# Optimization experiments

Measured on AMD Instinct MI355X. Metric: run time of the kernel, lower is better.

The kernel has to match this reference:

```python
import jax, jax.numpy as jnp
import numpy as np
from jax import lax

T, K, D = 2097152, 8, 4
LOG_2PI = float(np.log(2.0 * np.pi))


def setup_inputs() -> dict:
    key = jax.random.key(0)
    k1, k2, k3, k4 = jax.random.split(key, 4)
    return {
        "x_seq": jax.random.normal(k1, (T, D), dtype=jnp.float32),
        "unnormalized_trans": jax.random.normal(k2, (K, K), dtype=jnp.float32),
        "unnormalized_pi": jax.random.normal(k3, (K,), dtype=jnp.float32),
        "means": jax.random.normal(k4, (K, D), dtype=jnp.float32) * 0.01,
        "log_std": jnp.zeros((K, D), dtype=jnp.float32),
    }


def reference(x_seq, unnormalized_trans, unnormalized_pi, means, log_std):
    # Row-stochastic transition / initial distributions in log space
    log_trans = jax.nn.log_softmax(unnormalized_trans, axis=-1)  # [K, K]
    log_pi = jax.nn.log_softmax(unnormalized_pi, axis=-1)        # [K]

    # Diagonal-Gaussian log emission densities: [T, K]
    std = jnp.exp(log_std)                                        # [K, D]
    z = (x_seq[:, None, :] - means[None, :, :]) / std[None, :, :]  # [T, K, D]
    log_em = jnp.sum(-0.5 * LOG_2PI - log_std[None] - 0.5 * z * z, axis=-1)  # [T, K]

    # Forward algorithm in log space (strictly sequential recurrence)
    alpha0 = log_pi + log_em[0]  # [K]

    def step(alpha, em_t):
        # alpha[i] + log_trans[i, j], logsumexp over source state i
        alpha = em_t + jax.scipy.special.logsumexp(alpha[:, None] + log_trans, axis=0)
        return alpha, None

    alpha, _ = lax.scan(step, alpha0, log_em[1:])
    return jax.scipy.special.logsumexp(alpha, axis=0)
```

## Files before the change

kernel.cpp:

```cpp
#include <hip/hip_runtime.h>
#include <math.h>

#define T_LEN 2097152
#define K 8
#define D 4
#define CHUNK 8
#define TPB 64
#define NBLK (T_LEN / (CHUNK * TPB))
#define MS4 19
#define NMID 16
#define MPM (NBLK / NMID)

typedef float f2 __attribute__((ext_vector_type(2)));

__device__ __forceinline__ f2 fma2(f2 a, f2 b, f2 c) { return __builtin_elementwise_fma(a, b, c); }
__device__ __forceinline__ f2 max2(f2 a, f2 b) { return __builtin_elementwise_max(a, b); }
__device__ __forceinline__ f2 splat(float s) { f2 r; r.x = s; r.y = s; return r; }


__device__ __forceinline__ float4* matp4(float* lm, int li) {
    return reinterpret_cast<float4*>(lm) + li * MS4 + ((li >> 1) & 3);
}

__device__ __forceinline__ void renorm2(f2 M[K][4], float& shift) {
    f2 m2 = max2(max2(M[0][0], M[0][1]), max2(M[0][2], M[0][3]));
#pragma unroll
    for (int i = 1; i < K; ++i)
        m2 = max2(m2, max2(max2(M[i][0], M[i][1]), max2(M[i][2], M[i][3])));
    float mx = fmaxf(m2.x, m2.y);
    int ex = (__float_as_int(mx) >> 23) & 255;
    float scale = __int_as_float((254 - ex) << 23);
    shift += (float)(ex - 127);
    f2 sc = splat(scale);
#pragma unroll
    for (int i = 0; i < K; ++i)
#pragma unroll
        for (int jj = 0; jj < 4; ++jj) M[i][jj] = M[i][jj] * sc;
}

__device__ __forceinline__ void store_mat(float* lm, int li, const f2 M[K][4]) {
    float4* dst = matp4(lm, li);
#pragma unroll
    for (int i = 0; i < K; ++i) {
        float4 w0, w1;
        w0.x = M[i][0].x; w0.y = M[i][0].y; w0.z = M[i][1].x; w0.w = M[i][1].y;
        w1.x = M[i][2].x; w1.y = M[i][2].y; w1.z = M[i][3].x; w1.w = M[i][3].y;
        dst[i * 2] = w0;
        dst[i * 2 + 1] = w1;
    }
}

__device__ __forceinline__ void combine8(float* lm, float* lsh, int li, int ri, int i) {
    const float4* Lb = matp4(lm, li);
    const float4* Rb = matp4(lm, ri);
    float4 la = Lb[i * 2], lb = Lb[i * 2 + 1];
    float4 R[16];
#pragma unroll
    for (int q = 0; q < 16; ++q) R[q] = Rb[q];
    float lk[8] = {la.x, la.y, la.z, la.w, lb.x, lb.y, lb.z, lb.w};
    f2 acc[4];
#pragma unroll
    for (int k = 0; k < 8; ++k) {
        f2 s = splat(lk[k]);
        f2 r0, r1, r2_, r3;
        r0.x = R[2 * k].x;      r0.y = R[2 * k].y;
        r1.x = R[2 * k].z;      r1.y = R[2 * k].w;
        r2_.x = R[2 * k + 1].x; r2_.y = R[2 * k + 1].y;
        r3.x = R[2 * k + 1].z;  r3.y = R[2 * k + 1].w;
        if (k == 0) {
            acc[0] = s * r0; acc[1] = s * r1; acc[2] = s * r2_; acc[3] = s * r3;
        } else {
            acc[0] = fma2(s, r0, acc[0]); acc[1] = fma2(s, r1, acc[1]);
            acc[2] = fma2(s, r2_, acc[2]); acc[3] = fma2(s, r3, acc[3]);
        }
    }
    f2 m2 = max2(max2(acc[0], acc[1]), max2(acc[2], acc[3]));
    float mx = fmaxf(m2.x, m2.y);
    mx = fmaxf(mx, __shfl_xor(mx, 1));
    mx = fmaxf(mx, __shfl_xor(mx, 2));
    mx = fmaxf(mx, __shfl_xor(mx, 4));
    int ex = (__float_as_int(mx) >> 23) & 255;
    float scale = __int_as_float((254 - ex) << 23);
    float ns = lsh[li] + lsh[ri] + (float)(ex - 127);
    f2 sc = splat(scale);
    f2 o0 = acc[0] * sc, o1 = acc[1] * sc, o2 = acc[2] * sc, o3 = acc[3] * sc;
    float4 w0, w1;
    w0.x = o0.x; w0.y = o0.y; w0.z = o1.x; w0.w = o1.y;
    w1.x = o2.x; w1.y = o2.y; w1.z = o3.x; w1.w = o3.y;
    float4* Ob = matp4(lm, li);
    Ob[i * 2] = w0;
    Ob[i * 2 + 1] = w1;
    if (i == 0) lsh[li] = ns;
}

__device__ __forceinline__ void hybrid_tree64(f2 P2[K][4], float shift, float* lm, float* lsh) {
    const int t = threadIdx.x;
    const int g = t >> 3;
    const int i = t & 7;
    if ((t & 1) == 0) {
        store_mat(lm, t >> 1, P2);
        lsh[t >> 1] = shift;
    }
    __syncthreads();
    if (t & 1) {
        const float4* src = matp4(lm, t >> 1);
        float lsv = lsh[t >> 1];
        f2 C[K][4];
#pragma unroll
        for (int r = 0; r < K; ++r) {
            float4 la = src[r * 2], lb = src[r * 2 + 1];
            float lk[8] = {la.x, la.y, la.z, la.w, lb.x, lb.y, lb.z, lb.w};
            f2 q[4];
#pragma unroll
            for (int k = 0; k < 8; ++k) {
                f2 s = splat(lk[k]);
                if (k == 0) {
#pragma unroll
                    for (int jj = 0; jj < 4; ++jj) q[jj] = s * P2[k][jj];
                } else {
#pragma unroll
                    for (int jj = 0; jj < 4; ++jj) q[jj] = fma2(s, P2[k][jj], q[jj]);
                }
            }
#pragma unroll
            for (int jj = 0; jj < 4; ++jj) C[r][jj] = q[jj];
        }
        float ns = shift + lsv;
        renorm2(C, ns);
        store_mat(lm, t >> 1, C);
        lsh[t >> 1] = ns;
    }
    __syncthreads();
    combine8(lm, lsh, 2 * g, 2 * g + 1, i);
    combine8(lm, lsh, 2 * (g + 8), 2 * (g + 8) + 1, i);
    __syncthreads();
    combine8(lm, lsh, 4 * g, 4 * g + 2, i);
    __syncthreads();
    if (g < 4) combine8(lm, lsh, 8 * g, 8 * g + 4, i);
    __syncthreads();
    if (g < 2) combine8(lm, lsh, 16 * g, 16 * g + 8, i);
    __syncthreads();
    if (g < 1) combine8(lm, lsh, 0, 16, i);
    __syncthreads();
}

__device__ __forceinline__ void tree_levels256(float* lm, float* lsh) {
    const int g = threadIdx.x >> 3;
    const int i = threadIdx.x & 7;
#pragma unroll 1
    for (int lvl = 1; lvl <= 3; ++lvl) {
        const int c = 64 >> (lvl - 1);
        const int S = 1 << (lvl - 1);
#pragma unroll 1
        for (int m = g; m < c; m += 32) combine8(lm, lsh, 2 * m * S, 2 * m * S + S, i);
        __syncthreads();
    }
    if (threadIdx.x < 64) {
#pragma unroll 1
        for (int lvl = 4; lvl <= 7; ++lvl) {
            const int c = 64 >> (lvl - 1);
            const int S = 1 << (lvl - 1);
            if (g < c) combine8(lm, lsh, 2 * g * S, 2 * g * S + S, i);
            asm volatile("s_waitcnt lgkmcnt(0)" ::: "memory");
        }
    }
}

__device__ __forceinline__ void hybrid_tree256(f2 P2[K][4], float shift, float* lm, float* lsh) {
    const int t = threadIdx.x;
    if ((t & 1) == 0) {
        store_mat(lm, t >> 1, P2);
        lsh[t >> 1] = shift;
    }
    __syncthreads();
    if (t & 1) {
        const float4* src = matp4(lm, t >> 1);
        float lsv = lsh[t >> 1];
        f2 C[K][4];
#pragma unroll
        for (int r = 0; r < K; ++r) {
            float4 la = src[r * 2], lb = src[r * 2 + 1];
            float lk[8] = {la.x, la.y, la.z, la.w, lb.x, lb.y, lb.z, lb.w};
            f2 q[4];
#pragma unroll
            for (int k = 0; k < 8; ++k) {
                f2 s = splat(lk[k]);
                if (k == 0) {
#pragma unroll
                    for (int jj = 0; jj < 4; ++jj) q[jj] = s * P2[k][jj];
                } else {
#pragma unroll
                    for (int jj = 0; jj < 4; ++jj) q[jj] = fma2(s, P2[k][jj], q[jj]);
                }
            }
#pragma unroll
            for (int jj = 0; jj < 4; ++jj) C[r][jj] = q[jj];
        }
        float ns = shift + lsv;
        renorm2(C, ns);
        store_mat(lm, t >> 1, C);
        lsh[t >> 1] = ns;
    }
    __syncthreads();
    tree_levels256(lm, lsh);
}

__device__ __forceinline__ float emit_e2(const f2 ca2[4], const f2 cb2[4][4],
                                         const f2 cc2[4][4], float4 x, f2 e2[4]) {
    f2 x0 = splat(x.x), x1 = splat(x.y), x2 = splat(x.z), x3 = splat(x.w);
    f2 em2[4];
#pragma unroll
    for (int jj = 0; jj < 4; ++jj) {
        f2 t = ca2[jj];
        t = fma2(fma2(cc2[0][jj], x0, cb2[0][jj]), x0, t);
        t = fma2(fma2(cc2[1][jj], x1, cb2[1][jj]), x1, t);
        t = fma2(fma2(cc2[2][jj], x2, cb2[2][jj]), x2, t);
        t = fma2(fma2(cc2[3][jj], x3, cb2[3][jj]), x3, t);
        em2[jj] = t;
    }
    f2 m2 = max2(max2(em2[0], em2[1]), max2(em2[2], em2[3]));
    float me = fmaxf(m2.x, m2.y);
#pragma unroll
    for (int jj = 0; jj < 4; ++jj) {
        e2[jj].x = exp2f(em2[jj].x - me);
        e2[jj].y = exp2f(em2[jj].y - me);
    }
    return me;
}

__global__ void hmm_setup(const float* __restrict__ x,
                          const float* __restrict__ ut,
                          const float* __restrict__ up,
                          const float* __restrict__ mn,
                          const float* __restrict__ lsd,
                          float* __restrict__ ws) {
    const int lane = threadIdx.x;
    const float L2PI = 1.83787706640934548356f;
    const float LOG2E = 1.44269504088896340736f;

    if (lane == 0) reinterpret_cast<unsigned*>(ws + 152)[0] = 0u;

    float v = ut[lane];
    float m = v;
    m = fmaxf(m, __shfl_xor(m, 1));
    m = fmaxf(m, __shfl_xor(m, 2));
    m = fmaxf(m, __shfl_xor(m, 4));
    float e = expf(v - m);
    float s = e;
    s += __shfl_xor(s, 1); s += __shfl_xor(s, 2); s += __shfl_xor(s, 4);
    ws[lane] = e / s;

    float pv = up[lane & 7];
    float pm = pv;
    pm = fmaxf(pm, __shfl_xor(pm, 1));
    pm = fmaxf(pm, __shfl_xor(pm, 2));
    pm = fmaxf(pm, __shfl_xor(pm, 4));
    float pe = expf(pv - pm);
    float ps = pe;
    ps += __shfl_xor(ps, 1); ps += __shfl_xor(ps, 2); ps += __shfl_xor(ps, 4);
    float pival = pe / ps;

    int k = (lane & 31) >> 2, d = lane & 3;
    float lv = lsd[k * D + d];
    float mu = mn[k * D + d];
    float iv = expf(-2.f * lv);
    float bn = mu * iv;
    float cn = -0.5f * iv;
    float aterm = -0.5f * L2PI - lv - 0.5f * mu * mu * iv;
    float ak = aterm;
    ak += __shfl_xor(ak, 1); ak += __shfl_xor(ak, 2);
    if (lane < 32) {
        ws[72 + lane]  = bn * LOG2E;
        ws[104 + lane] = cn * LOG2E;
        if (d == 0) ws[64 + k] = ak * LOG2E;
    }

    float xd = x[d];
    float part = (cn * xd + bn) * xd + aterm;
    part += __shfl_xor(part, 1); part += __shfl_xor(part, 2);
    float pik = __shfl(pival, k);
    if (lane < 32 && d == 0) ws[136 + k] = pik * expf(part);
}

__global__ __launch_bounds__(TPB) void hmm_main(const float* __restrict__ x,
                                                const float* __restrict__ cst,
                                                float* __restrict__ bp,
                                                float* __restrict__ bs) {
    __shared__ __align__(16) float lm[32 * 76];
    __shared__ float lsh[32];
    const int tid = blockIdx.x * TPB + threadIdx.x;

    float Tr[K][K];
#pragma unroll
    for (int i = 0; i < K; ++i)
#pragma unroll
        for (int j = 0; j < K; ++j) Tr[i][j] = cst[i * K + j];
    f2 Tr2[K][4];
#pragma unroll
    for (int i = 0; i < K; ++i)
#pragma unroll
        for (int jj = 0; jj < 4; ++jj) { Tr2[i][jj].x = Tr[i][2 * jj]; Tr2[i][jj].y = Tr[i][2 * jj + 1]; }

    f2 ca2[4], cb2[4][4], cc2[4][4];
#pragma unroll
    for (int jj = 0; jj < 4; ++jj) {
        ca2[jj].x = cst[64 + 2 * jj]; ca2[jj].y = cst[64 + 2 * jj + 1];
#pragma unroll
        for (int d = 0; d < 4; ++d) {
            cb2[d][jj].x = cst[72 + (2 * jj) * 4 + d];  cb2[d][jj].y = cst[72 + (2 * jj + 1) * 4 + d];
            cc2[d][jj].x = cst[104 + (2 * jj) * 4 + d]; cc2[d][jj].y = cst[104 + (2 * jj + 1) * 4 + d];
        }
    }

    const float4* xv = reinterpret_cast<const float4*>(x) + (size_t)tid * CHUNK;
    float4 xr[CHUNK];
#pragma unroll
    for (int t = 0; t < CHUNK; ++t) xr[t] = xv[t];

    f2 T2[K][4];
    float shift;
    {
        f2 eB[4];
        float meB = emit_e2(ca2, cb2, cc2, xr[1], eB);
        if (tid == 0) {
#pragma unroll
            for (int i = 0; i < K; ++i) {
                f2 a0 = splat(cst[136 + i]);
#pragma unroll
                for (int jj = 0; jj < 4; ++jj) T2[i][jj] = a0 * Tr2[i][jj] * eB[jj];
            }
            shift = meB;
        } else {
            f2 eA[4];
            float meA = emit_e2(ca2, cb2, cc2, xr[0], eA);
#pragma unroll
            for (int i = 0; i < K; ++i) {
                f2 ei = splat((i & 1) ? eA[i >> 1].y : eA[i >> 1].x);
#pragma unroll
                for (int jj = 0; jj < 4; ++jj) T2[i][jj] = ei * Tr2[i][jj] * eB[jj];
            }
            shift = meA + meB;
        }
    }

#pragma unroll
    for (int p = 1; p < 4; ++p) {
        f2 eA[4], eB[4];
        float meA = emit_e2(ca2, cb2, cc2, xr[2 * p], eA);
        float meB = emit_e2(ca2, cb2, cc2, xr[2 * p + 1], eB);
        shift += meA + meB;
#pragma unroll
        for (int i = 0; i < K; ++i) {
            f2 r2[4];
#pragma unroll
            for (int kk = 0; kk < 4; ++kk) r2[kk] = T2[i][kk] * eA[kk];
            f2 u[4];
#pragma unroll
            for (int jj = 0; jj < 4; ++jj) u[jj] = splat(r2[0].x) * Tr2[0][jj];
#pragma unroll
            for (int k = 1; k < 8; ++k) {
                f2 rk = splat((k & 1) ? r2[k >> 1].y : r2[k >> 1].x);
#pragma unroll
                for (int jj = 0; jj < 4; ++jj) u[jj] = fma2(rk, Tr2[k][jj], u[jj]);
            }
#pragma unroll
            for (int jj = 0; jj < 4; ++jj) T2[i][jj] = u[jj] * eB[jj];
        }
    }

    if (tid != 0) {
#pragma unroll
        for (int jj = 0; jj < 4; ++jj) {
            f2 c[K];
#pragma unroll
            for (int k = 0; k < K; ++k) c[k] = T2[k][jj];
#pragma unroll
            for (int i = 0; i < K; ++i) {
                f2 a = splat(Tr[i][0]) * c[0];
#pragma unroll
                for (int k = 1; k < K; ++k) a = fma2(splat(Tr[i][k]), c[k], a);
                T2[i][jj] = a;
            }
        }
    }

    renorm2(T2, shift);

    hybrid_tree64(T2, shift, lm, lsh);

    if (threadIdx.x == 0) {
        float4* o4 = reinterpret_cast<float4*>(bp + (size_t)blockIdx.x * 64);
        const float4* l4 = reinterpret_cast<const float4*>(lm);
#pragma unroll
        for (int q = 0; q < 16; ++q) o4[q] = l4[q];
        bs[blockIdx.x] = lsh[0];
    }
}

__global__ __launch_bounds__(256) void hmm_mid(const float* __restrict__ bp,
                                               const float* __restrict__ bs,
                                               float* __restrict__ bp2,
                                               float* __restrict__ bs2,
                                               unsigned* __restrict__ cnt,
                                               float* __restrict__ out) {
    __shared__ __align__(16) float lm[128 * 76];
    __shared__ float lsh[128];
    __shared__ int lastflag;
    const int t = threadIdx.x;
    const int g8 = t >> 3, i8 = t & 7;

    f2 P2[K][4];
    {
        const float4* p4 = reinterpret_cast<const float4*>(bp + (size_t)(blockIdx.x * MPM + t) * 64);
#pragma unroll
        for (int r = 0; r < K; ++r) {
            float4 a = p4[2 * r], b = p4[2 * r + 1];
            P2[r][0].x = a.x; P2[r][0].y = a.y;
            P2[r][1].x = a.z; P2[r][1].y = a.w;
            P2[r][2].x = b.x; P2[r][2].y = b.y;
            P2[r][3].x = b.z; P2[r][3].y = b.w;
        }
    }
    float shift = bs[blockIdx.x * MPM + t];

    hybrid_tree256(P2, shift, lm, lsh);

    if (t == 0) {
        const float* l0 = lm;
#pragma unroll
        for (int q = 0; q < 64; ++q)
            __hip_atomic_store(&bp2[blockIdx.x * 64 + q], l0[q], __ATOMIC_RELAXED, __HIP_MEMORY_SCOPE_AGENT);
        __hip_atomic_store(&bs2[blockIdx.x], lsh[0], __ATOMIC_RELAXED, __HIP_MEMORY_SCOPE_AGENT);
        __threadfence();
        unsigned ticket = __hip_atomic_fetch_add(cnt, 1u, __ATOMIC_ACQ_REL, __HIP_MEMORY_SCOPE_AGENT);
        lastflag = (ticket == NMID - 1) ? 1 : 0;
    }
    __syncthreads();
    if (!lastflag) return;

    __threadfence();
    if (t < 128) {
        const int g = t >> 3, i = t & 7;
        float* rowp = reinterpret_cast<float*>(matp4(lm, g) + 2 * i);
#pragma unroll
        for (int c = 0; c < 8; ++c)
            rowp[c] = __hip_atomic_load(&bp2[g * 64 + i * 8 + c], __ATOMIC_RELAXED, __HIP_MEMORY_SCOPE_AGENT);
        if (i == 0) lsh[g] = __hip_atomic_load(&bs2[g], __ATOMIC_RELAXED, __HIP_MEMORY_SCOPE_AGENT);
    }
    __syncthreads();
    if (t < 64) combine8(lm, lsh, 2 * g8, 2 * g8 + 1, i8);
    __syncthreads();
    if (t < 32) combine8(lm, lsh, 4 * g8, 4 * g8 + 2, i8);
    __syncthreads();
    if (t < 16) combine8(lm, lsh, 8 * g8, 8 * g8 + 4, i8);
    __syncthreads();
    if (t < 8)  combine8(lm, lsh, 0, 8, i8);
    __syncthreads();

    if (t == 0) {
        double s = 0.0;
#pragma unroll
        for (int q = 0; q < 64; ++q) s += (double)lm[q];
        out[0] = (float)(log(s) + (double)lsh[0] * 0.69314718055994530942);
    }
}

extern "C" void kernel_launch(void* const* d_in, const int* in_sizes, int n_in,
                              void* d_out, int out_size, void* d_ws, size_t ws_size,
                              hipStream_t stream) {
    (void)in_sizes; (void)n_in; (void)out_size; (void)ws_size;
    const float* x  = (const float*)d_in[0];
    const float* ut = (const float*)d_in[1];
    const float* up = (const float*)d_in[2];
    const float* mn = (const float*)d_in[3];
    const float* ls = (const float*)d_in[4];
    float* ws  = (float*)d_ws;
    float* out = (float*)d_out;
    float* bp  = ws + 256;
    float* bs  = bp + (size_t)NBLK * 64;
    float* bp2 = bs + NBLK;
    float* bs2 = bp2 + (size_t)NMID * 64;
    unsigned* cnt = reinterpret_cast<unsigned*>(ws + 152);

    hmm_setup<<<1, 64, 0, stream>>>(x, ut, up, mn, ls, ws);
    hmm_main<<<NBLK, TPB, 0, stream>>>(x, ws, bp, bs);
    hmm_mid<<<NMID, 256, 0, stream>>>(bp, bs, bp2, bs2, cnt, out);
}
```

Measured before the change: 126.4 us.

## Replace multi-block mid reduction with single-block serial-then-tree reduce

The second-stage reduction no longer uses 16 blocks with an atomic ticket and last-block combine. A single 256-thread block now has each thread serially multiply 16 consecutive block matrices, prefetching the next one, and then runs the shared-memory tree. The change also swaps exp2f in the emission computation for the raw v_exp_f32 instruction and makes hmm_main write its result with all 64 threads instead of one. This removes the atomic counter, fences and extra combine pass, but the final stage now runs on only one CU with a longer serial chain per thread.

```diff
diff --git a/kernel.cpp b/kernel.cpp
--- a/kernel.cpp
+++ b/kernel.cpp
@@ -8,14 +8,19 @@
 #define TPB 64
 #define NBLK (T_LEN / (CHUNK * TPB))
 #define MS4 19
-#define NMID 16
-#define MPM (NBLK / NMID)
+#define RPT 16
 
 typedef float f2 __attribute__((ext_vector_type(2)));
 
 __device__ __forceinline__ f2 fma2(f2 a, f2 b, f2 c) { return __builtin_elementwise_fma(a, b, c); }
 __device__ __forceinline__ f2 max2(f2 a, f2 b) { return __builtin_elementwise_max(a, b); }
 __device__ __forceinline__ f2 splat(float s) { f2 r; r.x = s; r.y = s; return r; }
+
+__device__ __forceinline__ float exp2_raw(float x) {
+    float r;
+    asm("v_exp_f32 %0, %1" : "=v"(r) : "v"(x));
+    return r;
+}
 
 
 __device__ __forceinline__ float4* matp4(float* lm, int li) {
@@ -222,8 +227,8 @@
     float me = fmaxf(m2.x, m2.y);
 #pragma unroll
     for (int jj = 0; jj < 4; ++jj) {
-        e2[jj].x = exp2f(em2[jj].x - me);
-        e2[jj].y = exp2f(em2[jj].y - me);
+        e2[jj].x = exp2_raw(em2[jj].x - me);
+        e2[jj].y = exp2_raw(em2[jj].y - me);
     }
     return me;
 }
@@ -237,8 +242,6 @@
     const int lane = threadIdx.x;
     const float L2PI = 1.83787706640934548356f;
     const float LOG2E = 1.44269504088896340736f;
-
-    if (lane == 0) reinterpret_cast<unsigned*>(ws + 152)[0] = 0u;
 
     float v = ut[lane];
     float m = v;
@@ -288,7 +291,8 @@
                                                 float* __restrict__ bs) {
     __shared__ __align__(16) float lm[32 * 76];
     __shared__ float lsh[32];
-    const int tid = blockIdx.x * TPB + threadIdx.x;
+    const int t = threadIdx.x;
+    const int tid = blockIdx.x * TPB + t;
 
     float Tr[K][K];
 #pragma unroll
@@ -315,7 +319,7 @@
     const float4* xv = reinterpret_cast<const float4*>(x) + (size_t)tid * CHUNK;
     float4 xr[CHUNK];
 #pragma unroll
-    for (int t = 0; t < CHUNK; ++t) xr[t] = xv[t];
+    for (int q = 0; q < CHUNK; ++q) xr[q] = xv[q];
 
     f2 T2[K][4];
     float shift;
@@ -388,74 +392,81 @@
 
     hybrid_tree64(T2, shift, lm, lsh);
 
-    if (threadIdx.x == 0) {
-        float4* o4 = reinterpret_cast<float4*>(bp + (size_t)blockIdx.x * 64);
-        const float4* l4 = reinterpret_cast<const float4*>(lm);
-#pragma unroll
-        for (int q = 0; q < 16; ++q) o4[q] = l4[q];
-        bs[blockIdx.x] = lsh[0];
-    }
-}
-
-__global__ __launch_bounds__(256) void hmm_mid(const float* __restrict__ bp,
-                                               const float* __restrict__ bs,
-                                               float* __restrict__ bp2,
-                                               float* __restrict__ bs2,
-                                               unsigned* __restrict__ cnt,
-                                               float* __restrict__ out) {
+    bp[(size_t)blockIdx.x * 64 + t] = lm[t];
+    if (t == 0) bs[blockIdx.x] = lsh[0];
+}
+
+__global__ __launch_bounds__(256) void hmm_reduce(const float* __restrict__ bp,
+                                                  const float* __restrict__ bs,
+                                                  float* __restrict__ out) {
     __shared__ __align__(16) float lm[128 * 76];
     __shared__ float lsh[128];
-    __shared__ int lastflag;
     const int t = threadIdx.x;
-    const int g8 = t >> 3, i8 = t & 7;
+    const float4* base = reinterpret_cast<const float4*>(bp) + (size_t)t * RPT * 16;
 
     f2 P2[K][4];
     {
-        const float4* p4 = reinterpret_cast<const float4*>(bp + (size_t)(blockIdx.x * MPM + t) * 64);
+        float4 M0[16];
+#pragma unroll
+        for (int q = 0; q < 16; ++q) M0[q] = base[q];
 #pragma unroll
         for (int r = 0; r < K; ++r) {
-            float4 a = p4[2 * r], b = p4[2 * r + 1];
+            float4 a = M0[2 * r], b = M0[2 * r + 1];
             P2[r][0].x = a.x; P2[r][0].y = a.y;
             P2[r][1].x = a.z; P2[r][1].y = a.w;
             P2[r][2].x = b.x; P2[r][2].y = b.y;
             P2[r][3].x = b.z; P2[r][3].y = b.w;
         }
     }
-    float shift = bs[blockIdx.x * MPM + t];
+    float shift = bs[t * RPT];
+
+    float4 Rb[16];
+#pragma unroll
+    for (int q = 0; q < 16; ++q) Rb[q] = base[16 + q];
+
+#pragma unroll 1
+    for (int r = 1; r < RPT; ++r) {
+        float4 Rn[16];
+        if (r + 1 < RPT) {
+#pragma unroll
+            for (int q = 0; q < 16; ++q) Rn[q] = base[(r + 1) * 16 + q];
+        }
+        f2 C[K][4];
+#pragma unroll
+        for (int i = 0; i < K; ++i) {
+            f2 q[4];
+#pragma unroll
+            for (int k = 0; k < 8; ++k) {
+                float pk_ = (k & 1) ? P2[i][k >> 1].y : P2[i][k >> 1].x;
+                f2 s = splat(pk_);
+                f2 r0, r1, r2_, r3;
+                r0.x = Rb[2 * k].x;      r0.y = Rb[2 * k].y;
+                r1.x = Rb[2 * k].z;      r1.y = Rb[2 * k].w;
+                r2_.x = Rb[2 * k + 1].x; r2_.y = Rb[2 * k + 1].y;
+                r3.x = Rb[2 * k + 1].z;  r3.y = Rb[2 * k + 1].w;
+                if (k == 0) {
+                    q[0] = s * r0; q[1] = s * r1; q[2] = s * r2_; q[3] = s * r3;
+                } else {
+                    q[0] = fma2(s, r0, q[0]); q[1] = fma2(s, r1, q[1]);
+                    q[2] = fma2(s, r2_, q[2]); q[3] = fma2(s, r3, q[3]);
+                }
+            }
+#pragma unroll
+            for (int jj = 0; jj < 4; ++jj) C[i][jj] = q[jj];
+        }
+        shift += bs[t * RPT + r];
+        renorm2(C, shift);
+#pragma unroll
+        for (int i = 0; i < K; ++i)
+#pragma unroll
+            for (int jj = 0; jj < 4; ++jj) P2[i][jj] = C[i][jj];
+        if (r + 1 < RPT) {
+#pragma unroll
+            for (int q = 0; q < 16; ++q) Rb[q] = Rn[q];
+        }
+    }
 
     hybrid_tree256(P2, shift, lm, lsh);
-
-    if (t == 0) {
-        const float* l0 = lm;
-#pragma unroll
-        for (int q = 0; q < 64; ++q)
-            __hip_atomic_store(&bp2[blockIdx.x * 64 + q], l0[q], __ATOMIC_RELAXED, __HIP_MEMORY_SCOPE_AGENT);
-        __hip_atomic_store(&bs2[blockIdx.x], lsh[0], __ATOMIC_RELAXED, __HIP_MEMORY_SCOPE_AGENT);
-        __threadfence();
-        unsigned ticket = __hip_atomic_fetch_add(cnt, 1u, __ATOMIC_ACQ_REL, __HIP_MEMORY_SCOPE_AGENT);
-        lastflag = (ticket == NMID - 1) ? 1 : 0;
-    }
-    __syncthreads();
-    if (!lastflag) return;
-
-    __threadfence();
-    if (t < 128) {
-        const int g = t >> 3, i = t & 7;
-        float* rowp = reinterpret_cast<float*>(matp4(lm, g) + 2 * i);
-#pragma unroll
-        for (int c = 0; c < 8; ++c)
-            rowp[c] = __hip_atomic_load(&bp2[g * 64 + i * 8 + c], __ATOMIC_RELAXED, __HIP_MEMORY_SCOPE_AGENT);
-        if (i == 0) lsh[g] = __hip_atomic_load(&bs2[g], __ATOMIC_RELAXED, __HIP_MEMORY_SCOPE_AGENT);
-    }
-    __syncthreads();
-    if (t < 64) combine8(lm, lsh, 2 * g8, 2 * g8 + 1, i8);
-    __syncthreads();
-    if (t < 32) combine8(lm, lsh, 4 * g8, 4 * g8 + 2, i8);
-    __syncthreads();
-    if (t < 16) combine8(lm, lsh, 8 * g8, 8 * g8 + 4, i8);
-    __syncthreads();
-    if (t < 8)  combine8(lm, lsh, 0, 8, i8);
-    __syncthreads();
 
     if (t == 0) {
         double s = 0.0;
@@ -478,11 +489,8 @@
     float* out = (float*)d_out;
     float* bp  = ws + 256;
     float* bs  = bp + (size_t)NBLK * 64;
-    float* bp2 = bs + NBLK;
-    float* bs2 = bp2 + (size_t)NMID * 64;
-    unsigned* cnt = reinterpret_cast<unsigned*>(ws + 152);
 
     hmm_setup<<<1, 64, 0, stream>>>(x, ut, up, mn, ls, ws);
     hmm_main<<<NBLK, TPB, 0, stream>>>(x, ws, bp, bs);
-    hmm_mid<<<NMID, 256, 0, stream>>>(bp, bs, bp2, bs2, cnt, out);
-}
+    hmm_reduce<<<1, 256, 0, stream>>>(bp, bs, out);
+}
```

Result: slower. 143.7 us (+13.6%).
